# Optimization experiments

Hardware: AMD Instinct MI355X
Metric: run time of the kernel (lower is better)

Reference implementation:

```python
import jax, jax.numpy as jnp
import numpy as np

B, L, R, E, D = 16, 28, 64, 34, 512


def setup_inputs() -> dict:
    key = jax.random.key(0)
    ks = jax.random.split(key, 10)
    logits = jax.random.uniform(ks[0], (B, L, R), dtype=jnp.float32)
    evt_embeddings = jax.random.normal(ks[1], (B, 1, D), dtype=jnp.float32)
    arg_embeddings = jax.random.normal(ks[2], (B, L, D), dtype=jnp.float32)
    # valid-arg counts in [1, L] (used as mask-count multiplier and divisor)
    arg_padding_num = jax.random.randint(ks[3], (B,), 1, L + 1).astype(jnp.float32)
    evt_type_list = jax.random.randint(ks[4], (B,), 0, E)
    s = 1.0 / np.sqrt(D)
    WRT = jax.random.normal(ks[5], (R, D, D), dtype=jnp.float32) * s
    WTT = jax.random.normal(ks[6], (E, D, D), dtype=jnp.float32) * s
    w1 = jax.random.normal(ks[7], (D, 64), dtype=jnp.float32) * s
    b1 = jnp.zeros((64,), dtype=jnp.float32)
    w2 = jax.random.normal(ks[8], (64, 1), dtype=jnp.float32) * (1.0 / 8.0)
    b2 = jnp.zeros((1,), dtype=jnp.float32)
    return {"logits": logits, "evt_embeddings": evt_embeddings,
            "arg_embeddings": arg_embeddings, "arg_padding_num": arg_padding_num,
            "evt_type_list": evt_type_list, "WRT": WRT, "WTT": WTT,
            "w1": w1, "b1": b1, "w2": w2, "b2": b2}


def reference(logits, evt_embeddings, arg_embeddings, arg_padding_num,
              evt_type_list, WRT, WTT, w1, b1, w2, b2):
    # role transition matrix per (event, arg): one-hot/soft select over WRT
    # [B,L,R] x [R,D,D] -> [B,L,D,D]  (dominant, memory-bound intermediate)
    role_mats = jnp.einsum('blr,rde->blde', logits, WRT)
    # event transition matrix: one-hot select over WTT == gather
    evt_mats = WTT[evt_type_list]                      # [B,D,D]
    # event embedding transform: [B,1,D] bmm [B,D,D] -> [B,D]
    evt_trans = jnp.einsum('bd,bde->be', evt_embeddings[:, 0, :], evt_mats)
    # per-arg transform: [B,L,D] bmm [B,L,D,D] -> [B,L,D]
    role_trans = jnp.einsum('bld,blde->ble', arg_embeddings, role_mats)
    # multiply by count, sum over args, divide by count (as in the original)
    role_trans = role_trans * arg_padding_num[:, None, None]
    new_sum = jnp.sum(role_trans, axis=1)              # [B,D]
    div = new_sum / arg_padding_num[:, None]
    graph_embeddings = (div + evt_trans) / 2.0         # [B,D]
    # scorer MLP: Linear(D,64) -> ReLU -> Linear(64,1) -> Sigmoid
    h = jax.nn.relu(graph_embeddings @ w1 + b1)
    score = jax.nn.sigmoid(h @ w2 + b2)                # [B,1]
    return score
```

## Files before the change

kernel.cpp:

```cpp
#include <hip/hip_runtime.h>
#include <math.h>

#define BB 16
#define LL 28
#define RR 64
#define DD 512
#define KK (RR * DD)
#define NROLE 512
#define NEVT 128

__global__ void __launch_bounds__(256) kernel_a(
    const float* __restrict__ logits,
    const float* __restrict__ arg,
    const float* __restrict__ WRT,
    const float* __restrict__ WTT,
    const float* __restrict__ evt_emb,
    const int*   __restrict__ evt_type,
    float* __restrict__ part,
    float* __restrict__ evt_acc)
{
    __shared__ float smem[8192];
    const int t = threadIdx.x;

    if (blockIdx.x >= NROLE) {
        const int blk = blockIdx.x - NROLE;
        const int b  = blk >> 3;
        const int d0 = (blk & 7) * 64;
        const int ty = evt_type[b];
        const float* Wt = WTT + (size_t)ty * DD * DD;
        const int e4 = t & 127;
        const int s  = t >> 7;
        float4 a = {0.f, 0.f, 0.f, 0.f};
#pragma unroll 4
        for (int dd = s; dd < 64; dd += 2) {
            const int d = d0 + dd;
            const float em = evt_emb[b * DD + d];
            const float4 w = ((const float4*)(Wt + (size_t)d * DD))[e4];
            a.x = fmaf(em, w.x, a.x);
            a.y = fmaf(em, w.y, a.y);
            a.z = fmaf(em, w.z, a.z);
            a.w = fmaf(em, w.w, a.w);
        }
        atomicAdd(&evt_acc[b * DD + e4 * 4 + 0], a.x);
        atomicAdd(&evt_acc[b * DD + e4 * 4 + 1], a.y);
        atomicAdd(&evt_acc[b * DD + e4 * 4 + 2], a.z);
        atomicAdd(&evt_acc[b * DD + e4 * 4 + 3], a.w);
        return;
    }

    const int blk = blockIdx.x;
    const int r  = blk >> 3;
    const int d0 = (blk & 7) * 64;

    {
        const int dl = t & 63;
        const int b4 = t >> 6;
        float g0 = 0.f, g1 = 0.f, g2 = 0.f, g3 = 0.f;
        const int d = d0 + dl;
#pragma unroll
        for (int l = 0; l < LL; ++l) {
            const int b0 = b4 * 4;
            const float a0 = arg[((b0 + 0) * LL + l) * DD + d];
            const float a1 = arg[((b0 + 1) * LL + l) * DD + d];
            const float a2 = arg[((b0 + 2) * LL + l) * DD + d];
            const float a3 = arg[((b0 + 3) * LL + l) * DD + d];
            g0 = fmaf(logits[((b0 + 0) * LL + l) * RR + r], a0, g0);
            g1 = fmaf(logits[((b0 + 1) * LL + l) * RR + r], a1, g1);
            g2 = fmaf(logits[((b0 + 2) * LL + l) * RR + r], a2, g2);
            g3 = fmaf(logits[((b0 + 3) * LL + l) * RR + r], a3, g3);
        }
        ((float4*)smem)[dl * 4 + b4] = make_float4(g0, g1, g2, g3);
    }
    __syncthreads();

    const int e4 = t & 127;
    const int ks = t >> 7;
    const float4* Wp = (const float4*)(WRT + ((size_t)(r * DD + d0)) * DD);
    const float4* Gl = (const float4*)smem;
    float4 acc[16];
#pragma unroll
    for (int b = 0; b < 16; ++b) acc[b] = make_float4(0.f, 0.f, 0.f, 0.f);

#pragma unroll 2
    for (int kk = ks; kk < 64; kk += 2) {
        const float4 w = Wp[(size_t)kk * 128 + e4];
        float4 g[4];
        g[0] = Gl[kk * 4 + 0];
        g[1] = Gl[kk * 4 + 1];
        g[2] = Gl[kk * 4 + 2];
        g[3] = Gl[kk * 4 + 3];
        const float* gs = (const float*)g;
#pragma unroll
        for (int b = 0; b < 16; ++b) {
            acc[b].x = fmaf(gs[b], w.x, acc[b].x);
            acc[b].y = fmaf(gs[b], w.y, acc[b].y);
            acc[b].z = fmaf(gs[b], w.z, acc[b].z);
            acc[b].w = fmaf(gs[b], w.w, acc[b].w);
        }
    }
    __syncthreads();

    if (ks == 1) {
        float4* red = (float4*)smem;
#pragma unroll
        for (int b = 0; b < 16; ++b) red[(t - 128) * 16 + b] = acc[b];
    }
    __syncthreads();
    if (ks == 0) {
        const float4* red = (const float4*)smem;
        float4* po = (float4*)part + (size_t)blk * 2048;
#pragma unroll
        for (int b = 0; b < 16; ++b) {
            float4 o = acc[b];
            const float4 q = red[t * 16 + b];
            o.x += q.x; o.y += q.y; o.z += q.z; o.w += q.w;
            po[b * 128 + e4] = o;
        }
    }
}

__global__ void __launch_bounds__(256) kernel_reduce(
    const float* __restrict__ part,
    float* __restrict__ div_acc)
{
    const int ps = blockIdx.x & 31;
    const int oc = blockIdx.x >> 5;
    const int t  = threadIdx.x;
    const int o4 = oc * 256 + t;
    const float4* p4 = (const float4*)part;
    float4 s = {0.f, 0.f, 0.f, 0.f};
#pragma unroll
    for (int i = 0; i < 16; ++i) {
        const int p = ps * 16 + i;
        const float4 v = p4[(size_t)p * 2048 + o4];
        s.x += v.x; s.y += v.y; s.z += v.z; s.w += v.w;
    }
    atomicAdd(&div_acc[o4 * 4 + 0], s.x);
    atomicAdd(&div_acc[o4 * 4 + 1], s.y);
    atomicAdd(&div_acc[o4 * 4 + 2], s.z);
    atomicAdd(&div_acc[o4 * 4 + 3], s.w);
}

__global__ void __launch_bounds__(256) kernel_mlp(
    const float* __restrict__ div_acc,
    const float* __restrict__ evt_acc,
    const float* __restrict__ w1,
    const float* __restrict__ b1,
    const float* __restrict__ w2,
    const float* __restrict__ b2,
    float* __restrict__ out)
{
    __shared__ float hred[256];
    const int b  = blockIdx.x;
    const int t  = threadIdx.x;
    const int j  = t & 63;
    const int dq = t >> 6;
    float hp = 0.f;
#pragma unroll 8
    for (int i = 0; i < 128; ++i) {
        const int d = dq * 128 + i;
        const float g = (div_acc[b * DD + d] + evt_acc[b * DD + d]) * 0.5f;
        hp = fmaf(g, w1[d * 64 + j], hp);
    }
    hred[t] = hp;
    __syncthreads();
    if (t < 64) {
        float h = b1[j] + hred[j] + hred[64 + j] + hred[128 + j] + hred[192 + j];
        h = fmaxf(h, 0.f);
        float v = h * w2[j];
#pragma unroll
        for (int off = 32; off > 0; off >>= 1) v += __shfl_down(v, off, 64);
        if (j == 0) out[b] = 1.f / (1.f + expf(-(v + b2[0])));
    }
}

extern "C" void kernel_launch(void* const* d_in, const int* in_sizes, int n_in,
                              void* d_out, int out_size, void* d_ws, size_t ws_size,
                              hipStream_t stream) {
    const float* logits   = (const float*)d_in[0];
    const float* evt_emb  = (const float*)d_in[1];
    const float* arg_emb  = (const float*)d_in[2];
    const int*   evt_type = (const int*)d_in[4];
    const float* WRT      = (const float*)d_in[5];
    const float* WTT      = (const float*)d_in[6];
    const float* w1       = (const float*)d_in[7];
    const float* b1       = (const float*)d_in[8];
    const float* w2       = (const float*)d_in[9];
    const float* b2       = (const float*)d_in[10];
    float* out = (float*)d_out;

    float* part    = (float*)d_ws;
    float* div_acc = part + (size_t)NROLE * 8192;
    float* evt_acc = div_acc + BB * DD;

    hipMemsetAsync(div_acc, 0, 2 * BB * DD * sizeof(float), stream);

    hipLaunchKernelGGL(kernel_a, dim3(NROLE + NEVT), dim3(256), 0, stream,
                       logits, arg_emb, WRT, WTT, evt_emb, evt_type, part, evt_acc);
    hipLaunchKernelGGL(kernel_reduce, dim3(256), dim3(256), 0, stream,
                       part, div_acc);
    hipLaunchKernelGGL(kernel_mlp, dim3(BB), dim3(256), 0, stream,
                       div_acc, evt_acc, w1, b1, w2, b2, out);
}
```

Measured before the change: 166.7 us.

## Prefetch WRT tiles in registers and vectorize arg-projection loads

The role kernel now issues its first batch of WRT loads before computing the logits-weighted arg projection, so those global loads overlap with that phase. The GEMM loop software-pipelines by loading the next 8 float4 weight rows while computing the current ones. The arg projection switches to float4 loads with a transposed smem store, and the event path batches 8 loads ahead of its FMAs. The cost is higher register pressure (acc plus two 8-deep float4 buffers), which could lower occupancy or cause spills.

```diff
diff --git a/kernel.cpp b/kernel.cpp
--- a/kernel.cpp
+++ b/kernel.cpp
@@ -31,15 +31,23 @@
         const int e4 = t & 127;
         const int s  = t >> 7;
         float4 a = {0.f, 0.f, 0.f, 0.f};
-#pragma unroll 4
-        for (int dd = s; dd < 64; dd += 2) {
-            const int d = d0 + dd;
-            const float em = evt_emb[b * DD + d];
-            const float4 w = ((const float4*)(Wt + (size_t)d * DD))[e4];
-            a.x = fmaf(em, w.x, a.x);
-            a.y = fmaf(em, w.y, a.y);
-            a.z = fmaf(em, w.z, a.z);
-            a.w = fmaf(em, w.w, a.w);
+#pragma unroll
+        for (int db = 0; db < 64; db += 16) {
+            float  em[8];
+            float4 w[8];
+#pragma unroll
+            for (int i = 0; i < 8; ++i) {
+                const int d = d0 + db + s + 2 * i;
+                em[i] = evt_emb[b * DD + d];
+                w[i]  = ((const float4*)(Wt + (size_t)d * DD))[e4];
+            }
+#pragma unroll
+            for (int i = 0; i < 8; ++i) {
+                a.x = fmaf(em[i], w[i].x, a.x);
+                a.y = fmaf(em[i], w[i].y, a.y);
+                a.z = fmaf(em[i], w[i].z, a.z);
+                a.w = fmaf(em[i], w[i].w, a.w);
+            }
         }
         atomicAdd(&evt_acc[b * DD + e4 * 4 + 0], a.x);
         atomicAdd(&evt_acc[b * DD + e4 * 4 + 1], a.y);
@@ -52,51 +60,68 @@
     const int r  = blk >> 3;
     const int d0 = (blk & 7) * 64;
 
-    {
-        const int dl = t & 63;
-        const int b4 = t >> 6;
-        float g0 = 0.f, g1 = 0.f, g2 = 0.f, g3 = 0.f;
-        const int d = d0 + dl;
-#pragma unroll
-        for (int l = 0; l < LL; ++l) {
-            const int b0 = b4 * 4;
-            const float a0 = arg[((b0 + 0) * LL + l) * DD + d];
-            const float a1 = arg[((b0 + 1) * LL + l) * DD + d];
-            const float a2 = arg[((b0 + 2) * LL + l) * DD + d];
-            const float a3 = arg[((b0 + 3) * LL + l) * DD + d];
-            g0 = fmaf(logits[((b0 + 0) * LL + l) * RR + r], a0, g0);
-            g1 = fmaf(logits[((b0 + 1) * LL + l) * RR + r], a1, g1);
-            g2 = fmaf(logits[((b0 + 2) * LL + l) * RR + r], a2, g2);
-            g3 = fmaf(logits[((b0 + 3) * LL + l) * RR + r], a3, g3);
-        }
-        ((float4*)smem)[dl * 4 + b4] = make_float4(g0, g1, g2, g3);
-    }
-    __syncthreads();
-
     const int e4 = t & 127;
     const int ks = t >> 7;
     const float4* Wp = (const float4*)(WRT + ((size_t)(r * DD + d0)) * DD);
+
+    float4 w[8];
+#pragma unroll
+    for (int i = 0; i < 8; ++i)
+        w[i] = Wp[(size_t)(ks + 2 * i) * 128 + e4];
+
+    {
+        const int d4 = t & 15;
+        const int b  = t >> 4;
+        const float4* ap = (const float4*)(arg + d0) + d4;
+        float4 g = {0.f, 0.f, 0.f, 0.f};
+#pragma unroll
+        for (int l = 0; l < LL; ++l) {
+            const float lg = logits[(b * LL + l) * RR + r];
+            const float4 av = ap[(size_t)(b * LL + l) * 128];
+            g.x = fmaf(lg, av.x, g.x);
+            g.y = fmaf(lg, av.y, g.y);
+            g.z = fmaf(lg, av.z, g.z);
+            g.w = fmaf(lg, av.w, g.w);
+        }
+        smem[(4 * d4 + 0) * 16 + b] = g.x;
+        smem[(4 * d4 + 1) * 16 + b] = g.y;
+        smem[(4 * d4 + 2) * 16 + b] = g.z;
+        smem[(4 * d4 + 3) * 16 + b] = g.w;
+    }
+    __syncthreads();
+
     const float4* Gl = (const float4*)smem;
     float4 acc[16];
 #pragma unroll
     for (int b = 0; b < 16; ++b) acc[b] = make_float4(0.f, 0.f, 0.f, 0.f);
 
-#pragma unroll 2
-    for (int kk = ks; kk < 64; kk += 2) {
-        const float4 w = Wp[(size_t)kk * 128 + e4];
-        float4 g[4];
-        g[0] = Gl[kk * 4 + 0];
-        g[1] = Gl[kk * 4 + 1];
-        g[2] = Gl[kk * 4 + 2];
-        g[3] = Gl[kk * 4 + 3];
-        const float* gs = (const float*)g;
-#pragma unroll
-        for (int b = 0; b < 16; ++b) {
-            acc[b].x = fmaf(gs[b], w.x, acc[b].x);
-            acc[b].y = fmaf(gs[b], w.y, acc[b].y);
-            acc[b].z = fmaf(gs[b], w.z, acc[b].z);
-            acc[b].w = fmaf(gs[b], w.w, acc[b].w);
-        }
+#pragma unroll
+    for (int kb = 0; kb < 64; kb += 16) {
+        float4 wn[8];
+        if (kb + 16 < 64) {
+#pragma unroll
+            for (int i = 0; i < 8; ++i)
+                wn[i] = Wp[(size_t)(kb + 16 + ks + 2 * i) * 128 + e4];
+        }
+#pragma unroll
+        for (int i = 0; i < 8; ++i) {
+            const int kk = kb + ks + 2 * i;
+            float4 g[4];
+            g[0] = Gl[kk * 4 + 0];
+            g[1] = Gl[kk * 4 + 1];
+            g[2] = Gl[kk * 4 + 2];
+            g[3] = Gl[kk * 4 + 3];
+            const float* gs = (const float*)g;
+#pragma unroll
+            for (int b = 0; b < 16; ++b) {
+                acc[b].x = fmaf(gs[b], w[i].x, acc[b].x);
+                acc[b].y = fmaf(gs[b], w[i].y, acc[b].y);
+                acc[b].z = fmaf(gs[b], w[i].z, acc[b].z);
+                acc[b].w = fmaf(gs[b], w[i].w, acc[b].w);
+            }
+        }
+#pragma unroll
+        for (int i = 0; i < 8; ++i) w[i] = wn[i];
     }
     __syncthreads();
 
```

Result: faster. 162.2 us (-2.7%).
